# Optimization experiments

Measured on AMD Instinct MI355X. Metric: run time of the kernel, lower is better.

Reference implementation:

```python
import jax, jax.numpy as jnp
import numpy as np
import math

V, D, L, H, F, MAXLEN = 32000, 1024, 6, 16, 4096, 2048
B, S = 2, 2048
DK = D // H
EPS = 1e-5


def _ln(x, g, b):
    m = jnp.mean(x, axis=-1, keepdims=True)
    v = jnp.mean((x - m) ** 2, axis=-1, keepdims=True)
    return (x - m) / jnp.sqrt(v + EPS) * g + b


def setup_inputs() -> dict:
    key = jax.random.key(0)
    ks = jax.random.split(key, 12)
    std = 0.02
    inp = {
        "tokens": jax.random.randint(ks[0], (B, S), 0, V),
        "tok_emb": jax.random.normal(ks[1], (V, D), jnp.float32) * std,
        "pos_emb": jax.random.normal(ks[2], (MAXLEN, D), jnp.float32) * std,
        "Wq": jax.random.normal(ks[3], (L, D, D), jnp.float32) * std,
        "Wk": jax.random.normal(ks[4], (L, D, D), jnp.float32) * std,
        "Wv": jax.random.normal(ks[5], (L, D, D), jnp.float32) * std,
        "Wo": jax.random.normal(ks[6], (L, D, D), jnp.float32) * std,
        "ln1_g": jnp.ones((L, D), jnp.float32),
        "ln1_b": jnp.zeros((L, D), jnp.float32),
        "ln2_g": jnp.ones((L, D), jnp.float32),
        "ln2_b": jnp.zeros((L, D), jnp.float32),
        "W1": jax.random.normal(ks[7], (L, D, F), jnp.float32) * std,
        "b1": jnp.zeros((L, F), jnp.float32),
        "W2": jax.random.normal(ks[8], (L, F, D), jnp.float32) * std,
        "b2": jnp.zeros((L, D), jnp.float32),
        "lnf_g": jnp.ones((D,), jnp.float32),
        "lnf_b": jnp.zeros((D,), jnp.float32),
        "Wout": jax.random.normal(ks[9], (D, V), jnp.float32) * std,
    }
    return inp


def _block(x, Wq, Wk, Wv, Wo, ln1_g, ln1_b, ln2_g, ln2_b, W1, b1, W2, b2, mask):
    # causal multi-head attention (pre-LN)
    h = _ln(x, ln1_g, ln1_b)
    q = (h @ Wq).reshape(B, S, H, DK)
    k = (h @ Wk).reshape(B, S, H, DK)
    v = (h @ Wv).reshape(B, S, H, DK)
    scores = jnp.einsum("bqhd,bkhd->bhqk", q, k) / math.sqrt(DK)
    scores = jnp.where(mask, scores, -jnp.inf)
    attn = jax.nn.softmax(scores, axis=-1)
    ctx = jnp.einsum("bhqk,bkhd->bqhd", attn, v).reshape(B, S, D)
    x = x + ctx @ Wo
    # feed-forward
    h = _ln(x, ln2_g, ln2_b)
    h = jax.nn.gelu(h @ W1 + b1, approximate=False)
    x = x + h @ W2 + b2
    return x


def reference(tokens, tok_emb, pos_emb, Wq, Wk, Wv, Wo, ln1_g, ln1_b, ln2_g, ln2_b,
              W1, b1, W2, b2, lnf_g, lnf_b, Wout):
    x = tok_emb[tokens] + pos_emb[:S][None, :, :]  # [B,S,D]
    mask = jnp.tril(jnp.ones((S, S), bool))[None, None]  # [1,1,S,S]
    for l in range(L):
        x = _block(x, Wq[l], Wk[l], Wv[l], Wo[l], ln1_g[l], ln1_b[l],
                   ln2_g[l], ln2_b[l], W1[l], b1[l], W2[l], b2[l], mask)
    x = _ln(x, lnf_g, lnf_b)
    return x @ Wout  # [B,S,V] logits
```

## Files before the change

### kernel.cpp

```cpp
#include <hip/hip_runtime.h>
#include <stdint.h>

typedef unsigned short u16;
typedef __bf16 bf16x8 __attribute__((ext_vector_type(8)));
typedef u16   u16x8  __attribute__((ext_vector_type(8)));
typedef float f32x4  __attribute__((ext_vector_type(4)));

#define AS1(p) (const __attribute__((address_space(1))) void*)(p)
#define AS3(p) (__attribute__((address_space(3))) void*)(p)

__device__ __forceinline__ u16 f2b(float f){
  uint32_t u = __builtin_bit_cast(uint32_t, f);
  u = (u + 0x7FFFu + ((u >> 16) & 1u)) >> 16;
  return (u16)u;
}
__device__ __forceinline__ float fexp2(float x){
#if __has_builtin(__builtin_amdgcn_exp2f)
  return __builtin_amdgcn_exp2f(x);
#else
  return exp2f(x);
#endif
}

__global__ __launch_bounds__(256) void embed_k(const int* __restrict__ tokens,
                                               const float* __restrict__ te,
                                               const float* __restrict__ pe,
                                               float* __restrict__ x){
  const int n = blockIdx.x, tid = threadIdx.x;
  const int tok = tokens[n];
  float4 a = *(const float4*)&te[(size_t)tok * 1024 + tid * 4];
  const float4 p = *(const float4*)&pe[(size_t)(n & 2047) * 1024 + tid * 4];
  a.x += p.x; a.y += p.y; a.z += p.z; a.w += p.w;
  *(float4*)&x[(size_t)n * 1024 + tid * 4] = a;
}

__global__ __launch_bounds__(256) void ln_k(const float* __restrict__ x,
                                            const float* __restrict__ g,
                                            const float* __restrict__ b,
                                            u16* __restrict__ h){
  const int row = blockIdx.x, tid = threadIdx.x;
  const float4 v = *(const float4*)&x[(size_t)row * 1024 + tid * 4];
  float s = v.x + v.y + v.z + v.w;
  float q = v.x*v.x + v.y*v.y + v.z*v.z + v.w*v.w;
#pragma unroll
  for (int m = 32; m; m >>= 1){ s += __shfl_xor(s, m); q += __shfl_xor(q, m); }
  __shared__ float ss[4], qq[4];
  if ((tid & 63) == 0){ ss[tid >> 6] = s; qq[tid >> 6] = q; }
  __syncthreads();
  s = ss[0] + ss[1] + ss[2] + ss[3];
  q = qq[0] + qq[1] + qq[2] + qq[3];
  const float mean = s * (1.f/1024.f);
  const float var  = q * (1.f/1024.f) - mean*mean;
  const float rstd = rsqrtf(var + 1e-5f);
  const float4 gv = *(const float4*)&g[tid*4];
  const float4 bv = *(const float4*)&b[tid*4];
  ushort4 o;
  o.x = f2b((v.x-mean)*rstd*gv.x + bv.x);
  o.y = f2b((v.y-mean)*rstd*gv.y + bv.y);
  o.z = f2b((v.z-mean)*rstd*gv.z + bv.z);
  o.w = f2b((v.w-mean)*rstd*gv.w + bv.w);
  *(ushort4*)&h[(size_t)row * 1024 + tid * 4] = o;
}

__device__ __forceinline__ void conv_tile(const float* __restrict__ src,
                                          u16* __restrict__ dst,
                                          int R, int C, int bx, int by,
                                          u16 (*t)[72], int tid){
  const int r0 = by * 64, c0 = bx * 64;
  const int row = tid >> 4, col4 = tid & 15;
#pragma unroll
  for (int p = 0; p < 4; ++p){
    const int r = row + p * 16;
    const float4 v = *(const float4*)&src[(size_t)(r0 + r) * C + c0 + col4 * 4];
    t[r][col4*4+0] = f2b(v.x); t[r][col4*4+1] = f2b(v.y);
    t[r][col4*4+2] = f2b(v.z); t[r][col4*4+3] = f2b(v.w);
  }
  __syncthreads();
#pragma unroll
  for (int p = 0; p < 4; ++p){
    const int rr = row + p * 16;
    ushort4 w;
    w.x = t[col4*4+0][rr]; w.y = t[col4*4+1][rr];
    w.z = t[col4*4+2][rr]; w.w = t[col4*4+3][rr];
    *(ushort4*)&dst[(size_t)(c0 + rr) * R + r0 + col4 * 4] = w;
  }
}

__global__ __launch_bounds__(256) void conv_t(const float* __restrict__ src,
                                              u16* __restrict__ dst,
                                              int R, int C){
  __shared__ u16 t[64][72];
  conv_tile(src, dst, R, C, blockIdx.x, blockIdx.y, t, threadIdx.x);
}

__global__ __launch_bounds__(256) void conv6_k(const float* __restrict__ Wq,
                                               const float* __restrict__ Wk,
                                               const float* __restrict__ Wv,
                                               const float* __restrict__ Wo,
                                               const float* __restrict__ W1,
                                               const float* __restrict__ W2,
                                               u16* __restrict__ qkvT,
                                               u16* __restrict__ woT,
                                               u16* __restrict__ w1T,
                                               u16* __restrict__ w2T){
  __shared__ u16 t[64][72];
  const int id = blockIdx.x;
  const float* src; u16* dst; int R, C, bx, by;
  if (id < 1024){
    R = 1024; C = 1024;
    const int m = id >> 8, tt = id & 255; bx = tt & 15; by = tt >> 4;
    if (m == 0){ src = Wq; dst = qkvT; }
    else if (m == 1){ src = Wk; dst = qkvT + 1048576; }
    else if (m == 2){ src = Wv; dst = qkvT + 2097152; }
    else { src = Wo; dst = woT; }
  } else if (id < 2048){
    const int tt = id - 1024; R = 1024; C = 4096; bx = tt & 63; by = tt >> 6;
    src = W1; dst = w1T;
  } else {
    const int tt = id - 2048; R = 4096; C = 1024; bx = tt & 15; by = tt >> 4;
    src = W2; dst = w2T;
  }
  conv_tile(src, dst, R, C, bx, by, t, threadIdx.x);
}

template<int EPI>
__global__ __launch_bounds__(256) void gemm_bt(const u16* __restrict__ A,
                                               const u16* __restrict__ BT,
                                               void* __restrict__ Cout,
                                               const float* __restrict__ bias,
                                               int M, int N, int K){
  __shared__ __attribute__((aligned(16))) u16 As[128 * 64];
  __shared__ __attribute__((aligned(16))) u16 Bs[128 * 64];
  const int tid = threadIdx.x;
  const int lane = tid & 63, wave = tid >> 6;
  const int m0 = blockIdx.x * 128, n0 = blockIdx.y * 128;
  const int wm = wave >> 1, wn = wave & 1;
  const int l15 = lane & 15, l4 = lane >> 4;

  const int srow = tid >> 3;
  const int skb  = ((tid & 7) ^ (srow & 7)) * 8;
  const u16* Ag = A  + (size_t)(m0 + srow) * K + skb;
  const u16* Bg = BT + (size_t)(n0 + srow) * K + skb;
  char* AsB = (char*)As + wave * 1024;
  char* BsB = (char*)Bs + wave * 1024;

  f32x4 acc[4][4] = {};

  for (int k0 = 0; k0 < K; k0 += 64){
    __syncthreads();
#pragma unroll
    for (int c = 0; c < 4; ++c){
      __builtin_amdgcn_global_load_lds(AS1(Ag + (size_t)(c*32)*K + k0), AS3(AsB + c*4096), 16, 0, 0);
      __builtin_amdgcn_global_load_lds(AS1(Bg + (size_t)(c*32)*K + k0), AS3(BsB + c*4096), 16, 0, 0);
    }
    __syncthreads();
#pragma unroll
    for (int kk = 0; kk < 64; kk += 32){
      const int krd = kk + l4 * 8;
      const int kx  = (lane & 7) * 8;
      bf16x8 af[4], bfv[4];
#pragma unroll
      for (int mi = 0; mi < 4; ++mi){
        const int r = wm*64 + mi*16 + l15;
        af[mi] = *(const bf16x8*)&As[r*64 + (krd ^ kx)];
      }
#pragma unroll
      for (int ni = 0; ni < 4; ++ni){
        const int r = wn*64 + ni*16 + l15;
        bfv[ni] = *(const bf16x8*)&Bs[r*64 + (krd ^ kx)];
      }
#pragma unroll
      for (int mi = 0; mi < 4; ++mi)
#pragma unroll
        for (int ni = 0; ni < 4; ++ni)
          acc[mi][ni] = __builtin_amdgcn_mfma_f32_16x16x32_bf16(af[mi], bfv[ni], acc[mi][ni], 0, 0, 0);
    }
  }

#pragma unroll
  for (int mi = 0; mi < 4; ++mi){
    const int r = m0 + wm*64 + mi*16 + l4*4;
#pragma unroll
    for (int ni = 0; ni < 4; ++ni){
      const int c = n0 + wn*64 + ni*16 + l15;
      const f32x4 a = acc[mi][ni];
      if constexpr (EPI == 0){
        u16* C = (u16*)Cout;
#pragma unroll
        for (int j = 0; j < 4; ++j) C[(size_t)(r+j)*N + c] = f2b(a[j]);
      } else if constexpr (EPI == 1){
        float* C = (float*)Cout;
        const float bb = bias ? bias[c] : 0.f;
#pragma unroll
        for (int j = 0; j < 4; ++j){ const size_t o = (size_t)(r+j)*N + c; C[o] += a[j] + bb; }
      } else if constexpr (EPI == 2){
        u16* C = (u16*)Cout;
        const float bb = bias[c];
#pragma unroll
        for (int j = 0; j < 4; ++j){
          const float xv = a[j] + bb;
          C[(size_t)(r+j)*N + c] = f2b(0.5f * xv * (1.f + erff(xv * 0.70710678118654752f)));
        }
      } else {
        float* C = (float*)Cout;
#pragma unroll
        for (int j = 0; j < 4; ++j) C[(size_t)(r+j)*N + c] = a[j];
      }
    }
  }
}

__global__ __launch_bounds__(256) void attn_k(const u16* __restrict__ qkv,
                                              u16* __restrict__ ctx){
  __shared__ __attribute__((aligned(16))) u16 Ks[2][64*64];
  __shared__ __attribute__((aligned(16))) u16 Vt[2][64][72];
  __shared__ __attribute__((aligned(16))) u16 Ps[4][16][72];
  const int tid = threadIdx.x, lane = tid & 63, w = tid >> 6;
  const int l15 = lane & 15, l4 = lane >> 4;
  const int b = blockIdx.y >> 4, h = blockIdx.y & 15;
  const int bx = gridDim.x - 1 - blockIdx.x;
  const int q0 = bx * 64;
  const int qw = q0 + w * 16;
  const u16* qb = qkv + (size_t)b * 2048 * 3072 + h * 64;
  const u16* kb = qb + 1024;
  const u16* vb = qb + 2048;

  const bf16x8 qf0 = *(const bf16x8*)&qb[(size_t)(qw + l15) * 3072 + l4 * 8];
  const bf16x8 qf1 = *(const bf16x8*)&qb[(size_t)(qw + l15) * 3072 + 32 + l4 * 8];

  f32x4 o[4] = {};
  float mrun = -__builtin_inff(), lrun = 0.f;
  const float CEXP = 0.18033688f;

  const int T = bx + 1;
  const int vd = tid & 63, vkc = w;

  {
    u16* kd = &Ks[0][0];
#pragma unroll
    for (int s = 0; s < 2; ++s){
      const int r = s*32 + w*8 + (lane >> 3);
      __builtin_amdgcn_global_load_lds(AS1(kb + (size_t)r * 3072 + ((lane & 7) ^ (r & 7)) * 8),
                                       AS3(kd + (s*32 + w*8) * 64), 16, 0, 0);
    }
    u16 vr[16];
#pragma unroll
    for (int i = 0; i < 16; ++i) vr[i] = vb[(size_t)(vkc*16 + i) * 3072 + vd];
    u16x8 va, vb2;
#pragma unroll
    for (int i = 0; i < 8; ++i){ va[i] = vr[i]; vb2[i] = vr[8+i]; }
    *(u16x8*)&Vt[0][vd][vkc*16]     = va;
    *(u16x8*)&Vt[0][vd][vkc*16 + 8] = vb2;
  }
  __syncthreads();

  for (int t = 0; t < T; ++t){
    const int cur = t & 1;
    const int kt = t * 64;

    u16 vr[16];
    if (t + 1 < T){
      const int ktn = kt + 64;
      u16* kd = &Ks[cur ^ 1][0];
#pragma unroll
      for (int s = 0; s < 2; ++s){
        const int r = s*32 + w*8 + (lane >> 3);
        __builtin_amdgcn_global_load_lds(AS1(kb + (size_t)(ktn + r) * 3072 + ((lane & 7) ^ (r & 7)) * 8),
                                         AS3(kd + (s*32 + w*8) * 64), 16, 0, 0);
      }
#pragma unroll
      for (int i = 0; i < 16; ++i) vr[i] = vb[(size_t)(ktn + vkc*16 + i) * 3072 + vd];
    }

    f32x4 st[4] = {};
    __builtin_amdgcn_s_setprio(1);
#pragma unroll
    for (int t4 = 0; t4 < 4; ++t4){
      const int r = t4*16 + l15;
      const int sx = l15 & 7;
      const bf16x8 kf0 = *(const bf16x8*)&Ks[cur][r*64 + ((l4       ^ sx) * 8)];
      const bf16x8 kf1 = *(const bf16x8*)&Ks[cur][r*64 + (((4 + l4) ^ sx) * 8)];
      st[t4] = __builtin_amdgcn_mfma_f32_16x16x32_bf16(kf0, qf0, st[t4], 0, 0, 0);
      st[t4] = __builtin_amdgcn_mfma_f32_16x16x32_bf16(kf1, qf1, st[t4], 0, 0, 0);
    }
    __builtin_amdgcn_s_setprio(0);

    float sv[16];
#pragma unroll
    for (int t4 = 0; t4 < 4; ++t4)
#pragma unroll
      for (int j = 0; j < 4; ++j) sv[t4*4 + j] = st[t4][j];
    if (t == T - 1){
      const int qrow = qw + l15;
#pragma unroll
      for (int t4 = 0; t4 < 4; ++t4)
#pragma unroll
        for (int j = 0; j < 4; ++j){
          const int k = kt + t4*16 + l4*4 + j;
          if (k > qrow) sv[t4*4 + j] = -__builtin_inff();
        }
    }

    float x0 = fmaxf(fmaxf(sv[0],  sv[1]),  sv[2]);
    float x1 = fmaxf(fmaxf(sv[3],  sv[4]),  sv[5]);
    float x2 = fmaxf(fmaxf(sv[6],  sv[7]),  sv[8]);
    float x3 = fmaxf(fmaxf(sv[9],  sv[10]), sv[11]);
    float x4 = fmaxf(fmaxf(sv[12], sv[13]), sv[14]);
    float mt = fmaxf(fmaxf(fmaxf(x0, x1), x2), fmaxf(fmaxf(x3, x4), sv[15]));
    mt = fmaxf(mt, __shfl_xor(mt, 16));
    mt = fmaxf(mt, __shfl_xor(mt, 32));

    if (__any(mt > mrun + 64.f)){
      const float mn = fmaxf(mrun, mt);
      const float sc = fexp2((mrun - mn) * CEXP);
      lrun *= sc;
      mrun = mn;
#pragma unroll
      for (int j = 0; j < 4; ++j){
        const float scj = __shfl(sc, l4*4 + j);
        o[0][j] *= scj; o[1][j] *= scj; o[2][j] *= scj; o[3][j] *= scj;
      }
    }

    const float mb = -mrun * CEXP;
#pragma unroll
    for (int i = 0; i < 16; ++i) sv[i] = fexp2(__builtin_fmaf(sv[i], CEXP, mb));
    {
      float s0 = sv[0]+sv[1], s1 = sv[2]+sv[3], s2 = sv[4]+sv[5], s3 = sv[6]+sv[7];
      float s4 = sv[8]+sv[9], s5 = sv[10]+sv[11], s6 = sv[12]+sv[13], s7 = sv[14]+sv[15];
      float u0 = (s0+s1) + (s2+s3), u1 = (s4+s5) + (s6+s7);
      float rs = u0 + u1;
      rs += __shfl_xor(rs, 16);
      rs += __shfl_xor(rs, 32);
      lrun += rs;
    }

#pragma unroll
    for (int t4 = 0; t4 < 4; ++t4){
      uint32_t pk0, pk1;
      asm("v_cvt_pk_bf16_f32 %0, %1, %2" : "=v"(pk0) : "v"(sv[t4*4+0]), "v"(sv[t4*4+1]));
      asm("v_cvt_pk_bf16_f32 %0, %1, %2" : "=v"(pk1) : "v"(sv[t4*4+2]), "v"(sv[t4*4+3]));
      *(uint32_t*)&Ps[w][l15][t4*16 + l4*4]     = pk0;
      *(uint32_t*)&Ps[w][l15][t4*16 + l4*4 + 2] = pk1;
    }
    const bf16x8 pa0 = *(const bf16x8*)&Ps[w][l15][l4*8];
    const bf16x8 pa1 = *(const bf16x8*)&Ps[w][l15][32 + l4*8];

    __builtin_amdgcn_s_setprio(1);
#pragma unroll
    for (int dt = 0; dt < 4; ++dt){
      const bf16x8 vf0 = *(const bf16x8*)&Vt[cur][dt*16 + l15][l4*8];
      const bf16x8 vf1 = *(const bf16x8*)&Vt[cur][dt*16 + l15][32 + l4*8];
      o[dt] = __builtin_amdgcn_mfma_f32_16x16x32_bf16(pa0, vf0, o[dt], 0, 0, 0);
      o[dt] = __builtin_amdgcn_mfma_f32_16x16x32_bf16(pa1, vf1, o[dt], 0, 0, 0);
    }
    __builtin_amdgcn_s_setprio(0);

    if (t + 1 < T){
      u16x8 va, vb2;
#pragma unroll
      for (int i = 0; i < 8; ++i){ va[i] = vr[i]; vb2[i] = vr[8+i]; }
      *(u16x8*)&Vt[cur ^ 1][vd][vkc*16]     = va;
      *(u16x8*)&Vt[cur ^ 1][vd][vkc*16 + 8] = vb2;
    }
    __syncthreads();
  }

  const float inv = 1.f / lrun;
#pragma unroll
  for (int j = 0; j < 4; ++j){
    const float invj = __shfl(inv, l4*4 + j);
    u16* cb = ctx + (size_t)b * 2048 * 1024 + (size_t)(qw + l4*4 + j) * 1024 + h * 64;
#pragma unroll
    for (int dt = 0; dt < 4; ++dt)
      cb[dt*16 + l15] = f2b(o[dt][j] * invj);
  }
}

extern "C" void kernel_launch(void* const* d_in, const int* in_sizes, int n_in,
                              void* d_out, int out_size, void* d_ws, size_t ws_size,
                              hipStream_t stream){
  const int*   tokens = (const int*)d_in[0];
  const float* tok_emb= (const float*)d_in[1];
  const float* pos_emb= (const float*)d_in[2];
  const float* Wq  = (const float*)d_in[3];
  const float* Wk  = (const float*)d_in[4];
  const float* Wv  = (const float*)d_in[5];
  const float* Wo  = (const float*)d_in[6];
  const float* ln1g= (const float*)d_in[7];
  const float* ln1b= (const float*)d_in[8];
  const float* ln2g= (const float*)d_in[9];
  const float* ln2b= (const float*)d_in[10];
  const float* W1  = (const float*)d_in[11];
  const float* b1  = (const float*)d_in[12];
  const float* W2  = (const float*)d_in[13];
  const float* b2  = (const float*)d_in[14];
  const float* lnfg= (const float*)d_in[15];
  const float* lnfb= (const float*)d_in[16];
  const float* Wout= (const float*)d_in[17];

  char* ws = (char*)d_ws;
  float* x    = (float*)(ws + 0);
  u16*   h    = (u16*)(ws + 16777216);
  u16*   qkv  = (u16*)(ws + 25165824);
  u16*   ctxb = (u16*)(ws + 50331648);
  u16*   h1   = (u16*)(ws + 58720256);
  u16*   wT   = (u16*)(ws + 92274688);
  u16*   wqkvT= wT;
  u16*   woT  = wT + (size_t)3072 * 1024;
  u16*   w1T  = woT + (size_t)1024 * 1024;
  u16*   w2T  = w1T + (size_t)4096 * 1024;
  u16*   woutT= wT;

  embed_k<<<4096, 256, 0, stream>>>(tokens, tok_emb, pos_emb, x);

  for (int l = 0; l < 6; ++l){
    conv6_k<<<3072, 256, 0, stream>>>(Wq + (size_t)l*1048576, Wk + (size_t)l*1048576,
                                      Wv + (size_t)l*1048576, Wo + (size_t)l*1048576,
                                      W1 + (size_t)l*4194304, W2 + (size_t)l*4194304,
                                      wqkvT, woT, w1T, w2T);

    ln_k<<<4096, 256, 0, stream>>>(x, ln1g + l*1024, ln1b + l*1024, h);
    gemm_bt<0><<<dim3(32,24), 256, 0, stream>>>(h, wqkvT, qkv, nullptr, 4096, 3072, 1024);
    attn_k<<<dim3(32,32), 256, 0, stream>>>(qkv, ctxb);
    gemm_bt<1><<<dim3(32,8), 256, 0, stream>>>(ctxb, woT, x, nullptr, 4096, 1024, 1024);
    ln_k<<<4096, 256, 0, stream>>>(x, ln2g + l*1024, ln2b + l*1024, h);
    gemm_bt<2><<<dim3(32,32), 256, 0, stream>>>(h, w1T, h1, b1 + l*4096, 4096, 4096, 1024);
    gemm_bt<1><<<dim3(32,8), 256, 0, stream>>>(h1, w2T, x, b2 + l*1024, 4096, 1024, 4096);
  }

  ln_k<<<4096, 256, 0, stream>>>(x, lnfg, lnfb, h);
  conv_t<<<dim3(500,16), 256, 0, stream>>>(Wout, woutT, 1024, 32000);
  gemm_bt<3><<<dim3(32,250), 256, 0, stream>>>(h, woutT, (float*)d_out, nullptr, 4096, 32000, 1024);
}
```

Before: 2.529 ms.

## Add 256x256-tile, 512-thread triple-buffered GEMM for QKV, FFN1 and logits

Adds a new GEMM kernel with 256x256 output tiles per 512-thread block, a three-stage LDS ring filled by direct global-to-LDS loads, XOR-swizzled LDS reads, and a split-phase MFMA schedule with setprio. It replaces the old kernel for the QKV projection, the first FFN matmul and the output logits. The larger tiles raise arithmetic intensity and the deeper pipeline hides load latency. In exchange, grid counts drop (192 and 256 blocks on a 256-CU part), which risks poor CU fill and tail effects, and register pressure is high with 128 accumulator floats per lane.

```diff
diff --git a/kernel.cpp b/kernel.cpp
--- a/kernel.cpp
+++ b/kernel.cpp
@@ -210,6 +210,119 @@
   }
 }
 
+template<int EPI>
+__global__ __launch_bounds__(512) void gemm_bt2(const u16* __restrict__ A,
+                                                const u16* __restrict__ BT,
+                                                void* __restrict__ Cout,
+                                                const float* __restrict__ bias,
+                                                int M, int N, int K){
+  __shared__ __attribute__((aligned(16))) u16 Ls[3][2][256*32];
+  const int tid = threadIdx.x;
+  const int lane = tid & 63, wave = tid >> 6;
+  const int m0 = blockIdx.x * 256, n0 = blockIdx.y * 256;
+  const int wm = wave >> 2, wn = wave & 3;
+  const int l15 = lane & 15, l4 = lane >> 4;
+  const int kx = (l4 ^ (l15 & 3) ^ ((l15 >> 2) & 3)) * 8;
+  const int cg = ((lane & 3) ^ ((lane >> 2) & 3) ^ ((lane >> 4) & 3)) * 8;
+
+  const u16* Asrc = A  + (size_t)(m0 + wave*16 + (lane >> 2)) * K + cg;
+  const u16* Bsrc = BT + (size_t)(n0 + wave*16 + (lane >> 2)) * K + cg;
+  char* lds0 = (char*)&Ls[0][0][0];
+  const int wb = wave * 1024;
+
+#define STG(sb, k0, L) do{ \
+    __builtin_amdgcn_global_load_lds(AS1(Asrc + (size_t)((L)*128)*K + (size_t)(k0)), \
+        AS3(lds0 + (sb)*32768 +         (L)*8192 + wb), 16, 0, 0); \
+    __builtin_amdgcn_global_load_lds(AS1(Bsrc + (size_t)((L)*128)*K + (size_t)(k0)), \
+        AS3(lds0 + (sb)*32768 + 16384 + (L)*8192 + wb), 16, 0, 0); \
+  }while(0)
+
+  f32x4 acc[8][4] = {};
+  const int nt = K >> 5;
+
+  STG(0, 0, 0);  STG(0, 0, 1);
+  STG(1, 32, 0); STG(1, 32, 1);
+  asm volatile("s_waitcnt vmcnt(4)" ::: "memory");
+  __builtin_amdgcn_s_barrier();
+
+  int buf = 0;
+  for (int t = 0; t < nt; ++t){
+    const u16* LA = &Ls[buf][0][0];
+    const u16* LB = &Ls[buf][1][0];
+    int sb = buf + 2; if (sb >= 3) sb -= 3;
+    const int kn = (t + 2) << 5;
+    const bool st = (t + 2) < nt;
+
+    bf16x8 bf[4], af[4];
+#pragma unroll
+    for (int ni = 0; ni < 4; ++ni)
+      bf[ni] = *(const bf16x8*)&LB[(wn*64 + ni*16 + l15)*32 + kx];
+#pragma unroll
+    for (int mi = 0; mi < 4; ++mi)
+      af[mi] = *(const bf16x8*)&LA[(wm*128 + mi*16 + l15)*32 + kx];
+    if (st) STG(sb, kn, 0);
+    __builtin_amdgcn_s_barrier();
+    __builtin_amdgcn_s_setprio(1);
+#pragma unroll
+    for (int mi = 0; mi < 4; ++mi)
+#pragma unroll
+      for (int ni = 0; ni < 4; ++ni)
+        acc[mi][ni] = __builtin_amdgcn_mfma_f32_16x16x32_bf16(af[mi], bf[ni], acc[mi][ni], 0, 0, 0);
+    __builtin_amdgcn_s_setprio(0);
+    __builtin_amdgcn_s_barrier();
+
+#pragma unroll
+    for (int mi = 0; mi < 4; ++mi)
+      af[mi] = *(const bf16x8*)&LA[(wm*128 + (4+mi)*16 + l15)*32 + kx];
+    if (st) STG(sb, kn, 1);
+    __builtin_amdgcn_s_barrier();
+    __builtin_amdgcn_s_setprio(1);
+#pragma unroll
+    for (int mi = 0; mi < 4; ++mi)
+#pragma unroll
+      for (int ni = 0; ni < 4; ++ni)
+        acc[4+mi][ni] = __builtin_amdgcn_mfma_f32_16x16x32_bf16(af[mi], bf[ni], acc[4+mi][ni], 0, 0, 0);
+    __builtin_amdgcn_s_setprio(0);
+
+    if (t < nt - 2){
+      asm volatile("s_waitcnt vmcnt(4)" ::: "memory");
+      __builtin_amdgcn_s_barrier();
+    } else if (t == nt - 2){
+      asm volatile("s_waitcnt vmcnt(0)" ::: "memory");
+      __builtin_amdgcn_s_barrier();
+    }
+    buf = buf + 1; if (buf >= 3) buf -= 3;
+  }
+#undef STG
+
+#pragma unroll
+  for (int mi = 0; mi < 8; ++mi){
+    const int r = m0 + wm*128 + mi*16 + l4*4;
+#pragma unroll
+    for (int ni = 0; ni < 4; ++ni){
+      const int c = n0 + wn*64 + ni*16 + l15;
+      const f32x4 a = acc[mi][ni];
+      if constexpr (EPI == 0){
+        u16* C = (u16*)Cout;
+#pragma unroll
+        for (int j = 0; j < 4; ++j) C[(size_t)(r+j)*N + c] = f2b(a[j]);
+      } else if constexpr (EPI == 2){
+        u16* C = (u16*)Cout;
+        const float bb = bias[c];
+#pragma unroll
+        for (int j = 0; j < 4; ++j){
+          const float xv = a[j] + bb;
+          C[(size_t)(r+j)*N + c] = f2b(0.5f * xv * (1.f + erff(xv * 0.70710678118654752f)));
+        }
+      } else {
+        float* C = (float*)Cout;
+#pragma unroll
+        for (int j = 0; j < 4; ++j) C[(size_t)(r+j)*N + c] = a[j];
+      }
+    }
+  }
+}
+
 __global__ __launch_bounds__(256) void attn_k(const u16* __restrict__ qkv,
                                               u16* __restrict__ ctx){
   __shared__ __attribute__((aligned(16))) u16 Ks[2][64*64];
@@ -421,15 +534,15 @@
                                       wqkvT, woT, w1T, w2T);
 
     ln_k<<<4096, 256, 0, stream>>>(x, ln1g + l*1024, ln1b + l*1024, h);
-    gemm_bt<0><<<dim3(32,24), 256, 0, stream>>>(h, wqkvT, qkv, nullptr, 4096, 3072, 1024);
+    gemm_bt2<0><<<dim3(16,12), 512, 0, stream>>>(h, wqkvT, qkv, nullptr, 4096, 3072, 1024);
     attn_k<<<dim3(32,32), 256, 0, stream>>>(qkv, ctxb);
     gemm_bt<1><<<dim3(32,8), 256, 0, stream>>>(ctxb, woT, x, nullptr, 4096, 1024, 1024);
     ln_k<<<4096, 256, 0, stream>>>(x, ln2g + l*1024, ln2b + l*1024, h);
-    gemm_bt<2><<<dim3(32,32), 256, 0, stream>>>(h, w1T, h1, b1 + l*4096, 4096, 4096, 1024);
+    gemm_bt2<2><<<dim3(16,16), 512, 0, stream>>>(h, w1T, h1, b1 + l*4096, 4096, 4096, 1024);
     gemm_bt<1><<<dim3(32,8), 256, 0, stream>>>(h1, w2T, x, b2 + l*1024, 4096, 1024, 4096);
   }
 
   ln_k<<<4096, 256, 0, stream>>>(x, lnfg, lnfb, h);
   conv_t<<<dim3(500,16), 256, 0, stream>>>(Wout, woutT, 1024, 32000);
-  gemm_bt<3><<<dim3(32,250), 256, 0, stream>>>(h, woutT, (float*)d_out, nullptr, 4096, 32000, 1024);
-}
+  gemm_bt2<3><<<dim3(16,125), 512, 0, stream>>>(h, woutT, (float*)d_out, nullptr, 4096, 32000, 1024);
+}
```

Result: faster. 2.417 ms (-4.4%).
